# Optimization experiments

Hardware: AMD Instinct MI355X
Metric: run time of the kernel (lower is better)

Reference implementation:

```python
import jax, jax.numpy as jnp
import numpy as np

HEADS = 16
HEAD_DIM = 64  # embed_size // heads = 1024 // 16


def setup_inputs() -> dict:
    key = jax.random.key(0)
    ks = jax.random.split(key, 9)
    N, Sq, E, C = 4, 2048, 1024, 512
    Skv = 2 * Sq  # keys/values seq must equal doubled query seq (see view trick)
    return {
        "values": jax.random.normal(ks[0], (N, Skv, E), dtype=jnp.float32),
        "keys": jax.random.normal(ks[1], (N, Skv, E), dtype=jnp.float32),
        "queries": jax.random.normal(ks[2], (N, Sq, E), dtype=jnp.float32),
        "mask": jax.random.randint(ks[3], (N, Skv, HEADS, HEADS), 0, 2, dtype=jnp.int32),
        "condition": jax.random.normal(ks[4], (N, Sq, C), dtype=jnp.float32),
        "Wc": jax.random.normal(ks[5], (E, C), dtype=jnp.float32) * 0.02,
        "bc": jax.random.normal(ks[6], (E,), dtype=jnp.float32) * 0.02,
        "Wo": jax.random.normal(ks[7], (E, E), dtype=jnp.float32) * 0.02,
        "bo": jax.random.normal(ks[8], (E,), dtype=jnp.float32) * 0.02,
    }


def reference(values, keys, queries, mask, condition, Wc, bc, Wo, bo):
    N = queries.shape[0]
    H, D = HEADS, HEAD_DIM
    # condition_linear + concat: (N, Sq, 2E) -> view doubles seq -> (N, 2Sq, H, D)
    cond_feat = jnp.einsum('nsc,ec->nse', condition, Wc) + bc
    cq = jnp.concatenate([queries, cond_feat], axis=-1).reshape(N, -1, H, D)
    k = keys.reshape(N, -1, H, D)    # (N, 2Sq, H, D)
    v = values.reshape(N, -1, H, D)  # (N, 2Sq, H, D)
    # per-(batch,seq) heads-by-heads attention, exactly as the torch matmul does
    att = jnp.einsum('nshd,nsed->nshe', cq, k) / jnp.sqrt(jnp.float32(D))
    att = jnp.where(mask == 0, jnp.float32(-1e20), att)
    att = jax.nn.softmax(att, axis=-1)
    out = jnp.einsum('nshe,nsed->nshd', att, v).reshape(N, -1, H * D)
    return jnp.einsum('nsk,ek->nse', out, Wo) + bo
```

## Files before the change

kernel.cpp:

```cpp
#include <hip/hip_runtime.h>
#include <hip/hip_bf16.h>
#include <type_traits>

#define NB   4
#define SQ   2048
#define SKV  4096
#define EMB  1024
#define CDIM 512

typedef __attribute__((ext_vector_type(8))) short short8;
typedef __attribute__((ext_vector_type(4))) float f32x4;

__device__ __forceinline__ float b2f(ushort u) {
    union { unsigned int i; float f; } v;
    v.i = ((unsigned int)u) << 16;
    return v.f;
}
__device__ __forceinline__ ushort f2b(float f) {
    union { float f; unsigned int i; } v; v.f = f;
    unsigned int x = v.i;
    return (ushort)((x + 0x7fffu + ((x >> 16) & 1u)) >> 16);
}
__device__ __forceinline__ short8 pack_bf16x8(float4 a, float4 b) {
    union { short8 s; ushort u[8]; } r;
    r.u[0] = f2b(a.x); r.u[1] = f2b(a.y); r.u[2] = f2b(a.z); r.u[3] = f2b(a.w);
    r.u[4] = f2b(b.x); r.u[5] = f2b(b.y); r.u[6] = f2b(b.z); r.u[7] = f2b(b.w);
    return r.s;
}

__device__ __forceinline__ void glds16(const ushort* gp, ushort* lp) {
    __builtin_amdgcn_global_load_lds(
        (const __attribute__((address_space(1))) unsigned int*)gp,
        (__attribute__((address_space(3))) unsigned int*)lp,
        16, 0, 0);
}

__global__ __launch_bounds__(256)
void cvt_f32_bf16(const float* __restrict__ in, ushort* __restrict__ out, int n4)
{
    const int i = blockIdx.x * 256 + threadIdx.x;
    if (i < n4) {
        float4 v = ((const float4*)in)[i];
        ushort4 o;
        o.x = f2b(v.x); o.y = f2b(v.y); o.z = f2b(v.z); o.w = f2b(v.w);
        ((ushort4*)out)[i] = o;
    }
}

template <typename OT>
__global__ __launch_bounds__(256)
void gemm_bt_bias(const ushort* __restrict__ A, const ushort* __restrict__ B,
                  const float* __restrict__ bias, OT* __restrict__ C,
                  int M, int Nn, int K)
{
    __shared__ __attribute__((aligned(16))) ushort As[128 * 32];
    __shared__ __attribute__((aligned(16))) ushort Bs[128 * 32];

    const int tid  = threadIdx.x;
    const int wave = tid >> 6;
    const int lane = tid & 63;
    const int quad = lane >> 4;
    const int l16  = lane & 15;
    const int wr   = wave >> 1;
    const int wc   = wave & 1;

    const long mBase = (long)blockIdx.x * 128;
    const long nBase = (long)blockIdx.y * 128;

    const ushort* Ablk = A + mBase * K;
    const ushort* Bblk = B + nBase * K;

    const int lr = lane >> 2;
    const int lc = (lane & 3) * 8;
    const int c0 = wave * 2, c1 = wave * 2 + 1;
    const ushort* aG0 = Ablk + (long)(c0 * 16 + lr) * K + lc;
    const ushort* aG1 = Ablk + (long)(c1 * 16 + lr) * K + lc;
    const ushort* bG0 = Bblk + (long)(c0 * 16 + lr) * K + lc;
    const ushort* bG1 = Bblk + (long)(c1 * 16 + lr) * K + lc;
    ushort* aL0 = As + c0 * 512;
    ushort* aL1 = As + c1 * 512;
    ushort* bL0 = Bs + c0 * 512;
    ushort* bL1 = Bs + c1 * 512;

    f32x4 acc[4][4];
#pragma unroll
    for (int i = 0; i < 4; ++i)
#pragma unroll
        for (int j = 0; j < 4; ++j)
            acc[i][j] = (f32x4){0.f, 0.f, 0.f, 0.f};

    for (int k0 = 0; k0 < K; k0 += 32) {
        __syncthreads();
        glds16(aG0 + k0, aL0);
        glds16(aG1 + k0, aL1);
        glds16(bG0 + k0, bL0);
        glds16(bG1 + k0, bL1);
        __syncthreads();

        short8 af[4], bfr[4];
#pragma unroll
        for (int mt = 0; mt < 4; ++mt)
            af[mt] = *(const short8*)(As + (wr * 64 + mt * 16 + l16) * 32 + quad * 8);
#pragma unroll
        for (int nt = 0; nt < 4; ++nt)
            bfr[nt] = *(const short8*)(Bs + (wc * 64 + nt * 16 + l16) * 32 + quad * 8);

#pragma unroll
        for (int mt = 0; mt < 4; ++mt)
#pragma unroll
            for (int nt = 0; nt < 4; ++nt)
                acc[mt][nt] = __builtin_amdgcn_mfma_f32_16x16x32_bf16(
                    af[mt], bfr[nt], acc[mt][nt], 0, 0, 0);
    }

#pragma unroll
    for (int mt = 0; mt < 4; ++mt) {
#pragma unroll
        for (int nt = 0; nt < 4; ++nt) {
            const long n = nBase + wc * 64 + nt * 16 + l16;
            const float bv = bias[n];
#pragma unroll
            for (int r = 0; r < 4; ++r) {
                const long m = mBase + wr * 64 + mt * 16 + quad * 4 + r;
                if constexpr (std::is_same<OT, float>::value)
                    C[m * Nn + n] = acc[mt][nt][r] + bv;
                else
                    C[m * Nn + n] = f2b(acc[mt][nt][r] + bv);
            }
        }
    }
}

__global__ __launch_bounds__(256)
void attn_kernel(const float*  __restrict__ queries,
                 const ushort* __restrict__ condfeat,
                 const float*  __restrict__ keys,
                 const float*  __restrict__ values,
                 const int*    __restrict__ mask,
                 ushort* __restrict__ attout)
{
    const int wid  = threadIdx.x >> 6;
    const int pos  = blockIdx.x * 4 + wid;
    const int s2   = pos & 4095;
    const int n    = pos >> 12;
    const int lane = threadIdx.x & 63;
    const int quad = lane >> 4;
    const int l16  = lane & 15;

    short8 aF[2], bF[2];
    if (s2 & 1) {
        const ushort* cp = condfeat + ((size_t)n * SQ + (s2 >> 1)) * EMB
                           + l16 * 64 + quad * 8;
        aF[0] = *(const short8*)cp;
        aF[1] = *(const short8*)(cp + 32);
    } else {
        const float* qp = queries + ((size_t)n * SQ + (s2 >> 1)) * EMB
                          + l16 * 64 + quad * 8;
        aF[0] = pack_bf16x8(*(const float4*)qp,        *(const float4*)(qp + 4));
        aF[1] = pack_bf16x8(*(const float4*)(qp + 32), *(const float4*)(qp + 36));
    }
    {
        const float* kp = keys + (size_t)pos * EMB + l16 * 64 + quad * 8;
        bF[0] = pack_bf16x8(*(const float4*)kp,        *(const float4*)(kp + 4));
        bF[1] = pack_bf16x8(*(const float4*)(kp + 32), *(const float4*)(kp + 36));
    }

    f32x4 sc = (f32x4){0.f, 0.f, 0.f, 0.f};
    sc = __builtin_amdgcn_mfma_f32_16x16x32_bf16(aF[0], bF[0], sc, 0, 0, 0);
    sc = __builtin_amdgcn_mfma_f32_16x16x32_bf16(aF[1], bF[1], sc, 0, 0, 0);

    const int* mrow = mask + (size_t)pos * 256;
    float p[4];
#pragma unroll
    for (int r = 0; r < 4; ++r) {
        float s = sc[r] * 0.125f;
        const int mv = mrow[(quad * 4 + r) * 16 + l16];
        s = (mv == 0) ? -1e20f : s;
        float mx = s;
#pragma unroll
        for (int d = 1; d < 16; d <<= 1)
            mx = fmaxf(mx, __shfl_xor(mx, d));
        const float ex = __expf(s - mx);
        float sum = ex;
#pragma unroll
        for (int d = 1; d < 16; d <<= 1)
            sum += __shfl_xor(sum, d);
        p[r] = ex / sum;
    }

    float4 acc[4];
#pragma unroll
    for (int r = 0; r < 4; ++r) acc[r] = (float4){0.f, 0.f, 0.f, 0.f};

    const float* vp = values + (size_t)pos * EMB + l16 * 4;
#pragma unroll
    for (int eh = 0; eh < 2; ++eh) {
        float4 vv[8];
#pragma unroll
        for (int j = 0; j < 8; ++j)
            vv[j] = *(const float4*)(vp + (eh * 8 + j) * 64);
#pragma unroll
        for (int r = 0; r < 4; ++r) {
#pragma unroll
            for (int j = 0; j < 8; ++j) {
                const float pe = __shfl(p[r], quad * 16 + eh * 8 + j);
                acc[r].x += pe * vv[j].x;
                acc[r].y += pe * vv[j].y;
                acc[r].z += pe * vv[j].z;
                acc[r].w += pe * vv[j].w;
            }
        }
    }

    ushort* op = attout + (size_t)pos * EMB;
#pragma unroll
    for (int r = 0; r < 4; ++r) {
        ushort4 o;
        o.x = f2b(acc[r].x); o.y = f2b(acc[r].y);
        o.z = f2b(acc[r].z); o.w = f2b(acc[r].w);
        *(ushort4*)(op + (quad * 4 + r) * 64 + l16 * 4) = o;
    }
}

extern "C" void kernel_launch(void* const* d_in, const int* in_sizes, int n_in,
                              void* d_out, int out_size, void* d_ws, size_t ws_size,
                              hipStream_t stream)
{
    const float* values    = (const float*)d_in[0];
    const float* keys      = (const float*)d_in[1];
    const float* queries   = (const float*)d_in[2];
    const int*   mask      = (const int*)  d_in[3];
    const float* condition = (const float*)d_in[4];
    const float* Wc        = (const float*)d_in[5];
    const float* bc        = (const float*)d_in[6];
    const float* Wo        = (const float*)d_in[7];
    const float* bo        = (const float*)d_in[8];
    float* out = (float*)d_out;

    ushort* condfeat = (ushort*)d_ws;
    ushort* attout   = condfeat + (size_t)NB * SQ * EMB;
    ushort* cond_bf  = attout;
    ushort* Wc_bf    = attout + (size_t)NB * SQ * CDIM;
    ushort* Wo_bf    = condfeat;

    cvt_f32_bf16<<<(NB * SQ * CDIM / 4 + 255) / 256, 256, 0, stream>>>(
        condition, cond_bf, NB * SQ * CDIM / 4);
    cvt_f32_bf16<<<(EMB * CDIM / 4 + 255) / 256, 256, 0, stream>>>(
        Wc, Wc_bf, EMB * CDIM / 4);

    {
        dim3 grid((NB * SQ) / 128, EMB / 128);
        gemm_bt_bias<ushort><<<grid, 256, 0, stream>>>(
            cond_bf, Wc_bf, bc, condfeat, NB * SQ, EMB, CDIM);
    }

    attn_kernel<<<(NB * SKV) / 4, 256, 0, stream>>>(
        queries, condfeat, keys, values, mask, attout);

    cvt_f32_bf16<<<(EMB * EMB / 4 + 255) / 256, 256, 0, stream>>>(
        Wo, Wo_bf, EMB * EMB / 4);

    {
        dim3 grid((NB * SKV) / 128, EMB / 128);
        gemm_bt_bias<float><<<grid, 256, 0, stream>>>(
            attout, Wo_bf, bo, out, NB * SKV, EMB, EMB);
    }
}
```

Before: 309.2 us.

## Compute attention PV product with fp16 MFMA and transposed score layout

The score MFMA now computes the transposed product (keys as A, queries as B), so each lane holds four key entries for one query head. The softmax reduction then needs only two cross-lane shuffles, and the mask is read as a single int4. The probability-times-values product moves from shuffle-driven scalar FMAs to four fp16 16x16x16 MFMAs. All global loads (q, k, v, mask) are issued up front to overlap their latency. The trade-offs are fp16 rounding of probabilities and values, and scalar 2-byte output stores plus strided scalar value loads in place of vectorized ones.

```diff
diff --git a/kernel.cpp b/kernel.cpp
--- a/kernel.cpp
+++ b/kernel.cpp
@@ -10,6 +10,7 @@
 
 typedef __attribute__((ext_vector_type(8))) short short8;
 typedef __attribute__((ext_vector_type(4))) float f32x4;
+typedef __attribute__((ext_vector_type(4))) _Float16 half4;
 
 __device__ __forceinline__ float b2f(ushort u) {
     union { unsigned int i; float f; } v;
@@ -147,79 +148,80 @@
     const int quad = lane >> 4;
     const int l16  = lane & 15;
 
-    short8 aF[2], bF[2];
-    if (s2 & 1) {
+    short8 qF[2];
+    float4 qf[4];
+    const bool odd = (s2 & 1);
+    if (odd) {
         const ushort* cp = condfeat + ((size_t)n * SQ + (s2 >> 1)) * EMB
                            + l16 * 64 + quad * 8;
-        aF[0] = *(const short8*)cp;
-        aF[1] = *(const short8*)(cp + 32);
+        qF[0] = *(const short8*)cp;
+        qF[1] = *(const short8*)(cp + 32);
     } else {
         const float* qp = queries + ((size_t)n * SQ + (s2 >> 1)) * EMB
                           + l16 * 64 + quad * 8;
-        aF[0] = pack_bf16x8(*(const float4*)qp,        *(const float4*)(qp + 4));
-        aF[1] = pack_bf16x8(*(const float4*)(qp + 32), *(const float4*)(qp + 36));
-    }
-    {
-        const float* kp = keys + (size_t)pos * EMB + l16 * 64 + quad * 8;
-        bF[0] = pack_bf16x8(*(const float4*)kp,        *(const float4*)(kp + 4));
-        bF[1] = pack_bf16x8(*(const float4*)(kp + 32), *(const float4*)(kp + 36));
-    }
-
-    f32x4 sc = (f32x4){0.f, 0.f, 0.f, 0.f};
-    sc = __builtin_amdgcn_mfma_f32_16x16x32_bf16(aF[0], bF[0], sc, 0, 0, 0);
-    sc = __builtin_amdgcn_mfma_f32_16x16x32_bf16(aF[1], bF[1], sc, 0, 0, 0);
-
-    const int* mrow = mask + (size_t)pos * 256;
-    float p[4];
+        qf[0] = *(const float4*)qp;        qf[1] = *(const float4*)(qp + 4);
+        qf[2] = *(const float4*)(qp + 32); qf[3] = *(const float4*)(qp + 36);
+    }
+    const float* kp = keys + (size_t)pos * EMB + l16 * 64 + quad * 8;
+    float4 kf0 = *(const float4*)kp,        kf1 = *(const float4*)(kp + 4);
+    float4 kf2 = *(const float4*)(kp + 32), kf3 = *(const float4*)(kp + 36);
+    const float* vb = values + (size_t)pos * EMB;
+    float vf[4][4];
+#pragma unroll
+    for (int j = 0; j < 4; ++j)
+#pragma unroll
+        for (int dt = 0; dt < 4; ++dt)
+            vf[j][dt] = vb[(quad * 4 + j) * 64 + dt * 16 + l16];
+    const int4 m4 = *(const int4*)(mask + (size_t)pos * 256 + l16 * 16 + quad * 4);
+
+    short8 kF0 = pack_bf16x8(kf0, kf1);
+    short8 kF1 = pack_bf16x8(kf2, kf3);
+    if (!odd) {
+        qF[0] = pack_bf16x8(qf[0], qf[1]);
+        qF[1] = pack_bf16x8(qf[2], qf[3]);
+    }
+    f32x4 st = (f32x4){0.f, 0.f, 0.f, 0.f};
+    st = __builtin_amdgcn_mfma_f32_16x16x32_bf16(kF0, qF[0], st, 0, 0, 0);
+    st = __builtin_amdgcn_mfma_f32_16x16x32_bf16(kF1, qF[1], st, 0, 0, 0);
+
+    const int mv[4] = {m4.x, m4.y, m4.z, m4.w};
+    float s[4];
 #pragma unroll
     for (int r = 0; r < 4; ++r) {
-        float s = sc[r] * 0.125f;
-        const int mv = mrow[(quad * 4 + r) * 16 + l16];
-        s = (mv == 0) ? -1e20f : s;
-        float mx = s;
-#pragma unroll
-        for (int d = 1; d < 16; d <<= 1)
-            mx = fmaxf(mx, __shfl_xor(mx, d));
-        const float ex = __expf(s - mx);
-        float sum = ex;
-#pragma unroll
-        for (int d = 1; d < 16; d <<= 1)
-            sum += __shfl_xor(sum, d);
-        p[r] = ex / sum;
-    }
-
-    float4 acc[4];
-#pragma unroll
-    for (int r = 0; r < 4; ++r) acc[r] = (float4){0.f, 0.f, 0.f, 0.f};
-
-    const float* vp = values + (size_t)pos * EMB + l16 * 4;
-#pragma unroll
-    for (int eh = 0; eh < 2; ++eh) {
-        float4 vv[8];
-#pragma unroll
-        for (int j = 0; j < 8; ++j)
-            vv[j] = *(const float4*)(vp + (eh * 8 + j) * 64);
-#pragma unroll
-        for (int r = 0; r < 4; ++r) {
-#pragma unroll
-            for (int j = 0; j < 8; ++j) {
-                const float pe = __shfl(p[r], quad * 16 + eh * 8 + j);
-                acc[r].x += pe * vv[j].x;
-                acc[r].y += pe * vv[j].y;
-                acc[r].z += pe * vv[j].z;
-                acc[r].w += pe * vv[j].w;
-            }
-        }
+        float v = st[r] * 0.125f;
+        s[r] = (mv[r] == 0) ? -1e20f : v;
+    }
+    float mx = fmaxf(fmaxf(s[0], s[1]), fmaxf(s[2], s[3]));
+    mx = fmaxf(mx, __shfl_xor(mx, 16));
+    mx = fmaxf(mx, __shfl_xor(mx, 32));
+    float ex[4];
+    float sum = 0.f;
+#pragma unroll
+    for (int r = 0; r < 4; ++r) { ex[r] = __expf(s[r] - mx); sum += ex[r]; }
+    sum += __shfl_xor(sum, 16);
+    sum += __shfl_xor(sum, 32);
+    const float inv = 1.f / sum;
+
+    half4 pA;
+#pragma unroll
+    for (int r = 0; r < 4; ++r) pA[r] = (_Float16)(ex[r] * inv);
+
+    f32x4 oacc[4];
+#pragma unroll
+    for (int dt = 0; dt < 4; ++dt) {
+        half4 vF;
+#pragma unroll
+        for (int j = 0; j < 4; ++j) vF[j] = (_Float16)vf[j][dt];
+        f32x4 z = (f32x4){0.f, 0.f, 0.f, 0.f};
+        oacc[dt] = __builtin_amdgcn_mfma_f32_16x16x16f16(pA, vF, z, 0, 0, 0);
     }
 
     ushort* op = attout + (size_t)pos * EMB;
 #pragma unroll
-    for (int r = 0; r < 4; ++r) {
-        ushort4 o;
-        o.x = f2b(acc[r].x); o.y = f2b(acc[r].y);
-        o.z = f2b(acc[r].z); o.w = f2b(acc[r].w);
-        *(ushort4*)(op + (quad * 4 + r) * 64 + l16 * 4) = o;
-    }
+    for (int r = 0; r < 4; ++r)
+#pragma unroll
+        for (int dt = 0; dt < 4; ++dt)
+            op[(quad * 4 + r) * 64 + dt * 16 + l16] = f2b(oacc[dt][r]);
 }
 
 extern "C" void kernel_launch(void* const* d_in, const int* in_sizes, int n_in,
```

Result: no change. 306.1 us (-1.0%).
